# Kernel optimization log

Measured on AMD Instinct MI355X. Metric: run time of the kernel, lower is better.

## Reference

```python
import jax, jax.numpy as jnp
import numpy as np

EMBED_DIM = 1024
NUM_HEADS = 16
HEAD_DIM = EMBED_DIM // NUM_HEADS


def setup_inputs() -> dict:
    key = jax.random.key(0)
    k1, k2, k3, k4, k5 = jax.random.split(key, 5)
    B, T, C = 2, 2048, EMBED_DIM
    x = jax.random.normal(k1, (B, T, C), dtype=jnp.float32)
    # Linear params stored as (in, out) so y = x @ W + b
    s = 1.0 / np.sqrt(C)
    W_qkv = jax.random.uniform(k2, (C, 3 * C), minval=-s, maxval=s, dtype=jnp.float32)
    b_qkv = jax.random.uniform(k3, (3 * C,), minval=-s, maxval=s, dtype=jnp.float32)
    W_out = jax.random.uniform(k4, (C, C), minval=-s, maxval=s, dtype=jnp.float32)
    b_out = jax.random.uniform(k5, (C,), minval=-s, maxval=s, dtype=jnp.float32)
    return {"x": x, "W_qkv": W_qkv, "b_qkv": b_qkv, "W_out": W_out, "b_out": b_out}


def reference(x, W_qkv, b_qkv, W_out, b_out):
    B, T, C = x.shape
    H, D = NUM_HEADS, HEAD_DIM
    qkv = x @ W_qkv + b_qkv                       # [B, T, 3C]
    qkv = qkv.reshape(B, T, 3, H, D)
    q = qkv[:, :, 0].transpose(0, 2, 1, 3)        # [B, H, T, D]
    k = qkv[:, :, 1].transpose(0, 2, 1, 3)
    v = qkv[:, :, 2].transpose(0, 2, 1, 3)
    scores = jnp.einsum('bhqd,bhkd->bhqk', q, k) / jnp.sqrt(jnp.float32(D))
    causal = jnp.tril(jnp.ones((T, T), dtype=bool))
    scores = jnp.where(causal, scores, -jnp.inf)
    attn = jax.nn.softmax(scores, axis=-1)        # [B, H, T, T]
    out = jnp.einsum('bhqk,bhkd->bhqd', attn, v)  # [B, H, T, D]
    out = out.transpose(0, 2, 1, 3).reshape(B, T, C)
    out = out @ W_out + b_out
    return out
```

## Files before the change

kernel.cpp:

```cpp
#include <hip/hip_runtime.h>
#include <hip/hip_bf16.h>
#include <stdint.h>

typedef __bf16 bf16x8 __attribute__((ext_vector_type(8)));
typedef float  f32x4  __attribute__((ext_vector_type(4)));

typedef __attribute__((address_space(1))) void gas1_t;
typedef __attribute__((address_space(3))) void as3_t;

__device__ __forceinline__ void gload_lds16(const void* g, void* l) {
  __builtin_amdgcn_global_load_lds((gas1_t*)g, (as3_t*)l, 16, 0, 0);
}

__device__ __forceinline__ f32x4 zero4() { f32x4 z = {0.f, 0.f, 0.f, 0.f}; return z; }

__device__ __forceinline__ unsigned pack_bf16x2(float a, float b) {
  __bf16 ha = (__bf16)a, hb = (__bf16)b;
  unsigned short ua = *(unsigned short*)&ha, ub = *(unsigned short*)&hb;
  return (unsigned)ua | ((unsigned)ub << 16);
}

__device__ __forceinline__ float fast_exp2(float x) {
  float r;
  asm("v_exp_f32 %0, %1" : "=v"(r) : "v"(x));
  return r;
}

__global__ void cvt_f32_to_bf16(const float* __restrict__ in, __bf16* __restrict__ out, int n) {
  int i = (blockIdx.x * 256 + threadIdx.x) * 8;
  if (i >= n) return;
  const f32x4 v0 = *(const f32x4*)(in + i);
  const f32x4 v1 = *(const f32x4*)(in + i + 4);
  bf16x8 o;
#pragma unroll
  for (int j = 0; j < 4; ++j) { o[j] = (__bf16)v0[j]; o[j + 4] = (__bf16)v1[j]; }
  *(bf16x8*)(out + i) = o;
}

__global__ void transpose_cast(const float* __restrict__ W, __bf16* __restrict__ WT,
                               int K, int N) {
  __shared__ float tile[32][33];
  const int n0 = blockIdx.x * 32, k0 = blockIdx.y * 32;
  const int tx = threadIdx.x, ty = threadIdx.y;
  for (int i = ty; i < 32; i += 8) tile[i][tx] = W[(size_t)(k0 + i) * N + n0 + tx];
  __syncthreads();
  for (int i = ty; i < 32; i += 8) WT[(size_t)(n0 + i) * K + k0 + tx] = (__bf16)tile[tx][i];
}

template <int OUT_BF16, int A_F32, int SCALE_Q, int BN64>
__global__ __launch_bounds__(256) void gemm_bt(const void* __restrict__ Ap,
                                               const __bf16* __restrict__ BT,
                                               const float* __restrict__ bias,
                                               void* __restrict__ Cout,
                                               int M, int N, int K) {
  __shared__ __bf16 As[2][4096];
  __shared__ __bf16 Bs[2][BN64 ? 2048 : 4096];
  const int tid = threadIdx.x;
  const int lane = tid & 63, w = tid >> 6;
  const int wr = w >> 1, wc = w & 1;
  const int lgrp = lane >> 4, lcol = lane & 15;
  const int BN = BN64 ? 64 : 128;
  const int WCS = BN64 ? 32 : 64;
  const int NN = BN64 ? 2 : 4;
  const int m0 = blockIdx.y * 128, n0 = blockIdx.x * BN;

  f32x4 acc[4][BN64 ? 2 : 4];
#pragma unroll
  for (int m = 0; m < 4; ++m)
#pragma unroll
    for (int n = 0; n < NN; ++n) acc[m][n] = zero4();

  const int nk = K >> 5;

  auto stageB = [&](int buf, int k0) {
    if (BN64) {
      const int c = tid;
      const int row = c >> 2, kc = (c & 3) * 8;
      const int ldsoff = (w * 64) * 16;
      gload_lds16(BT + (size_t)(n0 + row) * K + k0 + kc, (char*)&Bs[buf][0] + ldsoff);
    } else {
#pragma unroll
      for (int q = 0; q < 2; ++q) {
        const int c = q * 256 + w * 64 + lane;
        const int row = c >> 2, kc = (c & 3) * 8;
        const int ldsoff = (q * 256 + w * 64) * 16;
        gload_lds16(BT + (size_t)(n0 + row) * K + k0 + kc, (char*)&Bs[buf][0] + ldsoff);
      }
    }
  };
  auto stageA = [&](int buf, int k0) {
    if (A_F32) {
      const float* A = (const float*)Ap;
      const int c0 = tid * 2;
      const int row = c0 >> 2, kc = (c0 & 3) * 8;
      const float* src = A + (size_t)(m0 + row) * K + k0 + kc;
      const f32x4 v0 = *(const f32x4*)(src);
      const f32x4 v1 = *(const f32x4*)(src + 4);
      const f32x4 v2 = *(const f32x4*)(src + 8);
      const f32x4 v3 = *(const f32x4*)(src + 12);
      bf16x8 o0, o1;
#pragma unroll
      for (int j = 0; j < 4; ++j) {
        o0[j] = (__bf16)v0[j]; o0[j + 4] = (__bf16)v1[j];
        o1[j] = (__bf16)v2[j]; o1[j + 4] = (__bf16)v3[j];
      }
      *(bf16x8*)((char*)&As[buf][0] + c0 * 16) = o0;
      *(bf16x8*)((char*)&As[buf][0] + c0 * 16 + 16) = o1;
    } else {
      const __bf16* A = (const __bf16*)Ap;
#pragma unroll
      for (int q = 0; q < 2; ++q) {
        const int c = q * 256 + w * 64 + lane;
        const int row = c >> 2, kc = (c & 3) * 8;
        const int ldsoff = (q * 256 + w * 64) * 16;
        gload_lds16(A + (size_t)(m0 + row) * K + k0 + kc, (char*)&As[buf][0] + ldsoff);
      }
    }
  };

  stageA(0, 0);
  stageB(0, 0);
  __syncthreads();
  int cur = 0;
  for (int t = 0; t < nk; ++t) {
    if (t + 1 < nk) { stageA(cur ^ 1, (t + 1) * 32); stageB(cur ^ 1, (t + 1) * 32); }
    bf16x8 af[4], bfr[BN64 ? 2 : 4];
#pragma unroll
    for (int m = 0; m < 4; ++m)
      af[m] = *(const bf16x8*)&As[cur][(wr * 64 + m * 16 + lcol) * 32 + lgrp * 8];
#pragma unroll
    for (int n = 0; n < NN; ++n)
      bfr[n] = *(const bf16x8*)&Bs[cur][(wc * WCS + n * 16 + lcol) * 32 + lgrp * 8];
    __builtin_amdgcn_s_setprio(1);
#pragma unroll
    for (int m = 0; m < 4; ++m)
#pragma unroll
      for (int n = 0; n < NN; ++n)
        acc[m][n] = __builtin_amdgcn_mfma_f32_16x16x32_bf16(af[m], bfr[n], acc[m][n], 0, 0, 0);
    __builtin_amdgcn_s_setprio(0);
    __syncthreads();
    cur ^= 1;
  }

#pragma unroll
  for (int m = 0; m < 4; ++m) {
#pragma unroll
    for (int n = 0; n < NN; ++n) {
      const int col = n0 + wc * WCS + n * 16 + lcol;
      const float bv = bias[col];
#pragma unroll
      for (int r = 0; r < 4; ++r) {
        const int row = m0 + wr * 64 + m * 16 + lgrp * 4 + r;
        float v = acc[m][n][r] + bv;
        if (SCALE_Q && col < 1024) v *= 0.18033688011112042f;
        if (OUT_BF16)
          ((__bf16*)Cout)[(size_t)row * N + col] = (__bf16)v;
        else
          ((float*)Cout)[(size_t)row * N + col] = v;
      }
    }
  }
}

__global__ __launch_bounds__(512, 4) void attn_fused(const __bf16* __restrict__ qkv,
                                                     __bf16* __restrict__ attnb) {
  __shared__ __bf16 Kl[2][64][80];
  __shared__ __bf16 Vt[2][64][80];
  __shared__ __bf16 Pl[8][16][144];
  const int tid = threadIdx.x, lane = tid & 63, w = tid >> 6;
  const int lgrp = lane >> 4, lcol = lane & 15;
  const int bh = blockIdx.y;
  const int xp = (bh & 16) ? (15 - blockIdx.x) : blockIdx.x;
  const int b = bh >> 4, h = bh & 15;
  const __bf16* base = qkv + (size_t)b * 2048 * 3072;

  const int qb = xp * 128;
  const int rw = qb + w * 16;
  const int nkv = xp + 1;

  const int krow = tid >> 3;
  const int d00 = (tid & 7) * 8;
  const int vcol = ((((krow >> 3) ^ (tid & 7)) << 3) | (krow & 7));
  const __bf16* kvp = base + 1024 + h * 64 + d00;

  const int q_l = rw + lcol;
  const __bf16* qptr = base + (size_t)q_l * 3072 + h * 64;
  const bf16x8 qf0 = *(const bf16x8*)(qptr + lgrp * 8);
  const bf16x8 qf1 = *(const bf16x8*)(qptr + 32 + lgrp * 8);

  float m1 = -1e30f, l1 = 0.f;
  f32x4 acc_o[4];
#pragma unroll
  for (int d = 0; d < 4; ++d) acc_o[d] = zero4();

  bf16x8 kf0 = *(const bf16x8*)(kvp + (size_t)krow * 3072);
  bf16x8 vf0 = *(const bf16x8*)(kvp + (size_t)krow * 3072 + 1024);
  bf16x8 kf1 = *(const bf16x8*)(kvp + (size_t)(krow + 64) * 3072);
  bf16x8 vf1 = *(const bf16x8*)(kvp + (size_t)(krow + 64) * 3072 + 1024);

  for (int kvb = 0; kvb < nkv; ++kvb) {
    const int kv0 = kvb * 128;
    __syncthreads();
    *(bf16x8*)&Kl[0][krow][d00] = kf0;
    *(bf16x8*)&Kl[1][krow][d00] = kf1;
#pragma unroll
    for (int j = 0; j < 8; ++j) {
      Vt[0][d00 + j][vcol] = vf0[j];
      Vt[1][d00 + j][vcol] = vf1[j];
    }
    __syncthreads();
    if (kvb + 1 < nkv) {
      const __bf16* p = kvp + (size_t)(kv0 + 128 + krow) * 3072;
      kf0 = *(const bf16x8*)p;
      vf0 = *(const bf16x8*)(p + 1024);
      kf1 = *(const bf16x8*)(p + (size_t)64 * 3072);
      vf1 = *(const bf16x8*)(p + (size_t)64 * 3072 + 1024);
    }

    const bool diag = (kvb == xp);
    const bool skip1 = diag && (w < 4);

    f32x4 accs[8];
    __builtin_amdgcn_s_setprio(1);
#pragma unroll
    for (int sub = 0; sub < 4; ++sub) {
      accs[sub] = zero4();
#pragma unroll
      for (int s = 0; s < 2; ++s) {
        const bf16x8 kb = *(const bf16x8*)&Kl[0][sub * 16 + lcol][s * 32 + lgrp * 8];
        accs[sub] = __builtin_amdgcn_mfma_f32_16x16x32_bf16(kb, s ? qf1 : qf0, accs[sub], 0, 0, 0);
      }
    }
    if (!skip1) {
#pragma unroll
      for (int sub = 0; sub < 4; ++sub) {
        accs[4 + sub] = zero4();
#pragma unroll
        for (int s = 0; s < 2; ++s) {
          const bf16x8 kb = *(const bf16x8*)&Kl[1][sub * 16 + lcol][s * 32 + lgrp * 8];
          accs[4 + sub] = __builtin_amdgcn_mfma_f32_16x16x32_bf16(kb, s ? qf1 : qf0, accs[4 + sub], 0, 0, 0);
        }
      }
    } else {
#pragma unroll
      for (int sub = 4; sub < 8; ++sub) accs[sub] = f32x4{-1e30f, -1e30f, -1e30f, -1e30f};
    }
    __builtin_amdgcn_s_setprio(0);

    if (diag) {
#pragma unroll
      for (int sub = 0; sub < 8; ++sub) {
        const int kvg = kv0 + sub * 16 + lgrp * 4;
#pragma unroll
        for (int r = 0; r < 4; ++r)
          if (kvg + r > q_l) accs[sub][r] = -1e30f;
      }
    }

    float mx[8];
#pragma unroll
    for (int sub = 0; sub < 8; ++sub)
      mx[sub] = fmaxf(fmaxf(accs[sub][0], accs[sub][1]), fmaxf(accs[sub][2], accs[sub][3]));
    float rm = fmaxf(fmaxf(fmaxf(mx[0], mx[1]), fmaxf(mx[2], mx[3])),
                     fmaxf(fmaxf(mx[4], mx[5]), fmaxf(mx[6], mx[7])));
    rm = fmaxf(rm, __shfl_xor(rm, 16));
    rm = fmaxf(rm, __shfl_xor(rm, 32));

    if (!__all(rm - m1 <= 8.0f)) {
      const float nm = fmaxf(m1, rm);
      const float sf = fast_exp2(m1 - nm);
      m1 = nm;
      l1 *= sf;
#pragma unroll
      for (int d = 0; d < 4; ++d)
#pragma unroll
        for (int r = 0; r < 4; ++r) acc_o[d][r] *= sf;
    }

    float ps[8];
#pragma unroll
    for (int sub = 0; sub < 8; ++sub) {
#pragma unroll
      for (int r = 0; r < 4; ++r) accs[sub][r] = fast_exp2(accs[sub][r] - m1);
      ps[sub] = (accs[sub][0] + accs[sub][1]) + (accs[sub][2] + accs[sub][3]);
    }
    float rs = ((ps[0] + ps[1]) + (ps[2] + ps[3])) + ((ps[4] + ps[5]) + (ps[6] + ps[7]));
    rs += __shfl_xor(rs, 16);
    rs += __shfl_xor(rs, 32);
    l1 += rs;

#pragma unroll
    for (int sub = 0; sub < 4; ++sub) {
      uint2 pk;
      pk.x = pack_bf16x2(accs[sub][0], accs[sub][1]);
      pk.y = pack_bf16x2(accs[sub][2], accs[sub][3]);
      const int eoff = ((((sub * 2 + (lgrp >> 1)) ^ ((lcol >> 2) & 3)) << 3) | ((lgrp & 1) << 2));
      *(uint2*)&Pl[w][lcol][eoff] = pk;
    }
    if (!skip1) {
#pragma unroll
      for (int sub = 4; sub < 8; ++sub) {
        uint2 pk;
        pk.x = pack_bf16x2(accs[sub][0], accs[sub][1]);
        pk.y = pack_bf16x2(accs[sub][2], accs[sub][3]);
        const int eoff = ((((sub * 2 + (lgrp >> 1)) ^ ((lcol >> 2) & 3)) << 3) | ((lgrp & 1) << 2));
        *(uint2*)&Pl[w][lcol][eoff] = pk;
      }
    }
    asm volatile("s_waitcnt lgkmcnt(0)" ::: "memory");
    __builtin_amdgcn_sched_barrier(0);
    __builtin_amdgcn_s_setprio(1);
#pragma unroll
    for (int s = 0; s < 2; ++s) {
      const bf16x8 pf = *(const bf16x8*)&Pl[w][lcol][((4 * s + lgrp) ^ ((lcol >> 2) & 3)) * 8];
#pragma unroll
      for (int d = 0; d < 4; ++d) {
        const bf16x8 vfr = *(const bf16x8*)&Vt[0][d * 16 + lcol][((4 * s + lgrp) ^ ((2 * d + (lcol >> 3)) & 7)) * 8];
        acc_o[d] = __builtin_amdgcn_mfma_f32_16x16x32_bf16(vfr, pf, acc_o[d], 0, 0, 0);
      }
    }
    if (!skip1) {
#pragma unroll
      for (int s = 2; s < 4; ++s) {
        const bf16x8 pf = *(const bf16x8*)&Pl[w][lcol][((4 * s + lgrp) ^ ((lcol >> 2) & 3)) * 8];
#pragma unroll
        for (int d = 0; d < 4; ++d) {
          const bf16x8 vfr = *(const bf16x8*)&Vt[1][d * 16 + lcol][((4 * (s - 2) + lgrp) ^ ((2 * d + (lcol >> 3)) & 7)) * 8];
          acc_o[d] = __builtin_amdgcn_mfma_f32_16x16x32_bf16(vfr, pf, acc_o[d], 0, 0, 0);
        }
      }
    }
    __builtin_amdgcn_s_setprio(0);
  }

  const float inv_l = 1.0f / l1;
  __bf16* orow = attnb + (size_t)(b * 2048 + q_l) * 1024 + h * 64 + lgrp * 4;
#pragma unroll
  for (int d = 0; d < 4; ++d) {
    uint2 ov;
    ov.x = pack_bf16x2(acc_o[d][0] * inv_l, acc_o[d][1] * inv_l);
    ov.y = pack_bf16x2(acc_o[d][2] * inv_l, acc_o[d][3] * inv_l);
    *(uint2*)(orow + d * 16) = ov;
  }
}

extern "C" void kernel_launch(void* const* d_in, const int* in_sizes, int n_in,
                              void* d_out, int out_size, void* d_ws, size_t ws_size,
                              hipStream_t stream) {
  const float* x    = (const float*)d_in[0];
  const float* Wqkv = (const float*)d_in[1];
  const float* bqkv = (const float*)d_in[2];
  const float* Wout = (const float*)d_in[3];
  const float* bout = (const float*)d_in[4];
  float* out = (float*)d_out;

  char* ws = (char*)d_ws;
  __bf16* qkvb  = (__bf16*)(ws);
  __bf16* wqkvT = (__bf16*)(ws + (24u << 20));
  __bf16* xb    = (__bf16*)(ws + (30u << 20));
  __bf16* attnb = (__bf16*)(ws + (24u << 20));
  __bf16* woutT = (__bf16*)(ws);

  const bool big_ws = ws_size >= ((size_t)38 << 20);

  transpose_cast<<<dim3(3072 / 32, 1024 / 32), dim3(32, 8), 0, stream>>>(Wqkv, wqkvT, 1024, 3072);

  if (big_ws) {
    cvt_f32_to_bf16<<<dim3(4096 * 1024 / 2048), dim3(256), 0, stream>>>(x, xb, 4096 * 1024);
    gemm_bt<1, 0, 1, 0><<<dim3(3072 / 128, 4096 / 128), dim3(256), 0, stream>>>(
        (const void*)xb, wqkvT, bqkv, (void*)qkvb, 4096, 3072, 1024);
  } else {
    gemm_bt<1, 1, 1, 0><<<dim3(3072 / 128, 4096 / 128), dim3(256), 0, stream>>>(
        (const void*)x, wqkvT, bqkv, (void*)qkvb, 4096, 3072, 1024);
  }

  attn_fused<<<dim3(16, 2 * 16), dim3(512), 0, stream>>>(qkvb, attnb);

  transpose_cast<<<dim3(1024 / 32, 1024 / 32), dim3(32, 8), 0, stream>>>(Wout, woutT, 1024, 1024);

  gemm_bt<0, 0, 0, 1><<<dim3(1024 / 64, 4096 / 128), dim3(256), 0, stream>>>(
      (const void*)attnb, woutT, bout, (void*)out, 4096, 1024, 1024);
}
```

Baseline: 120.0 us.

## Merge weight/activation prep into one kernel and use narrower QKV GEMM tiles

Combines the x fp32-to-bf16 cast and both weight transpose-casts into a single prep_all launch, which removes two kernel launches and the serialization gaps between them. Wout is placed at its own workspace offset so it can be prepared up front, and this raises the workspace threshold for the fast path. The QKV GEMM switches to 64-wide N tiles, which doubles its grid size to improve occupancy and wave balance on the many CUs, at the cost of less B-tile reuse per block.

```diff
diff --git a/kernel.cpp b/kernel.cpp
--- a/kernel.cpp
+++ b/kernel.cpp
@@ -45,6 +45,37 @@
   for (int i = ty; i < 32; i += 8) tile[i][tx] = W[(size_t)(k0 + i) * N + n0 + tx];
   __syncthreads();
   for (int i = ty; i < 32; i += 8) WT[(size_t)(n0 + i) * K + k0 + tx] = (__bf16)tile[tx][i];
+}
+
+__global__ __launch_bounds__(256) void prep_all(const float* __restrict__ x, __bf16* __restrict__ xb,
+                                                const float* __restrict__ Wqkv, __bf16* __restrict__ wqkvT,
+                                                const float* __restrict__ Wout, __bf16* __restrict__ woutT) {
+  const int bid = blockIdx.x;
+  if (bid < 2048) {
+    const int i = (bid * 256 + threadIdx.x) * 8;
+    const f32x4 v0 = *(const f32x4*)(x + i);
+    const f32x4 v1 = *(const f32x4*)(x + i + 4);
+    bf16x8 o;
+#pragma unroll
+    for (int j = 0; j < 4; ++j) { o[j] = (__bf16)v0[j]; o[j + 4] = (__bf16)v1[j]; }
+    *(bf16x8*)(xb + i) = o;
+    return;
+  }
+  __shared__ float tile[32][33];
+  const int tx = threadIdx.x & 31, ty = threadIdx.x >> 5;
+  const float* W; __bf16* WT; int N, n0, k0;
+  if (bid < 5120) {
+    const int l = bid - 2048;
+    W = Wqkv; WT = wqkvT; N = 3072;
+    n0 = (l % 96) * 32; k0 = (l / 96) * 32;
+  } else {
+    const int l = bid - 5120;
+    W = Wout; WT = woutT; N = 1024;
+    n0 = (l & 31) * 32; k0 = (l >> 5) * 32;
+  }
+  for (int i = ty; i < 32; i += 8) tile[i][tx] = W[(size_t)(k0 + i) * N + n0 + tx];
+  __syncthreads();
+  for (int i = ty; i < 32; i += 8) WT[(size_t)(n0 + i) * 1024 + k0 + tx] = (__bf16)tile[tx][i];
 }
 
 template <int OUT_BF16, int A_F32, int SCALE_Q, int BN64>
@@ -359,25 +390,25 @@
   __bf16* wqkvT = (__bf16*)(ws + (24u << 20));
   __bf16* xb    = (__bf16*)(ws + (30u << 20));
   __bf16* attnb = (__bf16*)(ws + (24u << 20));
-  __bf16* woutT = (__bf16*)(ws);
-
-  const bool big_ws = ws_size >= ((size_t)38 << 20);
-
-  transpose_cast<<<dim3(3072 / 32, 1024 / 32), dim3(32, 8), 0, stream>>>(Wqkv, wqkvT, 1024, 3072);
+
+  const bool big_ws = ws_size >= ((size_t)40 << 20);
 
   if (big_ws) {
-    cvt_f32_to_bf16<<<dim3(4096 * 1024 / 2048), dim3(256), 0, stream>>>(x, xb, 4096 * 1024);
-    gemm_bt<1, 0, 1, 0><<<dim3(3072 / 128, 4096 / 128), dim3(256), 0, stream>>>(
+    __bf16* woutT = (__bf16*)(ws + (38u << 20));
+    prep_all<<<dim3(2048 + 3072 + 1024), dim3(256), 0, stream>>>(x, xb, Wqkv, wqkvT, Wout, woutT);
+    gemm_bt<1, 0, 1, 1><<<dim3(3072 / 64, 4096 / 128), dim3(256), 0, stream>>>(
         (const void*)xb, wqkvT, bqkv, (void*)qkvb, 4096, 3072, 1024);
+    attn_fused<<<dim3(16, 2 * 16), dim3(512), 0, stream>>>(qkvb, attnb);
+    gemm_bt<0, 0, 0, 1><<<dim3(1024 / 64, 4096 / 128), dim3(256), 0, stream>>>(
+        (const void*)attnb, woutT, bout, (void*)out, 4096, 1024, 1024);
   } else {
+    __bf16* woutT = (__bf16*)(ws);
+    transpose_cast<<<dim3(3072 / 32, 1024 / 32), dim3(32, 8), 0, stream>>>(Wqkv, wqkvT, 1024, 3072);
     gemm_bt<1, 1, 1, 0><<<dim3(3072 / 128, 4096 / 128), dim3(256), 0, stream>>>(
         (const void*)x, wqkvT, bqkv, (void*)qkvb, 4096, 3072, 1024);
-  }
-
-  attn_fused<<<dim3(16, 2 * 16), dim3(512), 0, stream>>>(qkvb, attnb);
-
-  transpose_cast<<<dim3(1024 / 32, 1024 / 32), dim3(32, 8), 0, stream>>>(Wout, woutT, 1024, 1024);
-
-  gemm_bt<0, 0, 0, 1><<<dim3(1024 / 64, 4096 / 128), dim3(256), 0, stream>>>(
-      (const void*)attnb, woutT, bout, (void*)out, 4096, 1024, 1024);
-}
+    attn_fused<<<dim3(16, 2 * 16), dim3(512), 0, stream>>>(qkvb, attnb);
+    transpose_cast<<<dim3(1024 / 32, 1024 / 32), dim3(32, 8), 0, stream>>>(Wout, woutT, 1024, 1024);
+    gemm_bt<0, 0, 0, 1><<<dim3(1024 / 64, 4096 / 128), dim3(256), 0, stream>>>(
+        (const void*)attnb, woutT, bout, (void*)out, 4096, 1024, 1024);
+  }
+}
```

After: 127.8 us. 6.5% more time.
